# Kernel optimization log

Hardware: AMD Instinct MI355X
Metric: run time of the kernel (lower is better)

The kernel has to match this reference:

```python
import jax, jax.numpy as jnp
import numpy as np
import math

N = 512      # sequence length (residues)
CS = 384     # single_embedding_size
CZ = 128     # pair_embedding_size
C = 16       # ipa_embedding_size
PQ = 4       # num_query_points
PV = 8       # num_value_points
H = 12       # num_heads

SCALE_SINGLE = 1.0 / math.sqrt(C)
SCALE_FRAME = -1.0 / math.sqrt(18 * PQ)


def setup_inputs() -> dict:
    key = jax.random.key(0)
    ks = jax.random.split(key, 14)
    w = lambda k, shape: jax.random.normal(k, shape, dtype=jnp.float32) * 0.02
    return {
        "single_rep": jax.random.normal(ks[0], (N, CS), dtype=jnp.float32),
        "pair_rep": jax.random.normal(ks[1], (N, N, CZ), dtype=jnp.float32),
        "rotations": jax.random.normal(ks[2], (N, 3, 3), dtype=jnp.float32),
        "translations": jax.random.normal(ks[3], (N, 3), dtype=jnp.float32),
        "Wq": w(ks[4], (CS, H * C)),
        "Wk": w(ks[5], (CS, H * C)),
        "Wv": w(ks[6], (CS, H * C)),
        "Wqp": w(ks[7], (CS, H * PQ * 3)),
        "Wkp": w(ks[8], (CS, H * PQ * 3)),
        "Wvp": w(ks[9], (CS, H * PV * 3)),
        "Wb": w(ks[10], (CZ, H)),
        "Wout": w(ks[11], (H * (CZ + C + PV * 4), CS)),
        "bout": jnp.zeros((CS,), dtype=jnp.float32),
        "scale_head": jnp.ones((H,), dtype=jnp.float32),
    }


def reference(single_rep, pair_rep, rotations, translations,
              Wq, Wk, Wv, Wqp, Wkp, Wvp, Wb, Wout, bout, scale_head):
    n = single_rep.shape[0]

    def apply_frames(x):  # x: [n, h, p, 3] -> R_n x + t_n
        return jnp.einsum('nij,nhpj->nhpi', rotations, x) + translations[:, None, None, :]

    # projections
    q = (single_rep @ Wq).reshape(n, H, C)
    k = (single_rep @ Wk).reshape(n, H, C)
    v = (single_rep @ Wv).reshape(n, H, C)
    qp = (single_rep @ Wqp).reshape(n, H, PQ, 3)
    kp = (single_rep @ Wkp).reshape(n, H, PQ, 3)
    vp = (single_rep @ Wvp).reshape(n, H, PV, 3)

    # single-rep weight: [n, H, n]
    w_single = SCALE_SINGLE * jnp.einsum('nhc,mhc->nhm', q, k)

    # pair-rep bias weight: [n, H, n]
    w_pair = jnp.einsum('nmz,zh->nhm', pair_rep, Wb)

    # frame (point) weight
    lq = apply_frames(qp)  # [n,H,PQ,3]
    lk = apply_frames(kp)  # [n,H,PQ,3]
    diff = lq[:, None] - lk[None, :]                 # [n,n,H,PQ,3]
    d2 = jnp.sum(diff * diff, axis=(-1, -2))         # [n,n,H]
    w_frame = SCALE_FRAME * jax.nn.softplus(scale_head)[None, :, None] \
              * jnp.transpose(d2, (0, 2, 1))         # [n,H,n]

    weight = jax.nn.softmax(w_single + w_pair + w_frame, axis=-1)  # [n,H,n]

    # attentions
    o_single = jnp.einsum('nhm,mhc->nhc', weight, v)            # [n,H,C]
    o_pair = jnp.einsum('nhm,nmz->nhz', weight, pair_rep)       # [n,H,CZ]

    lvp = apply_frames(vp)                                      # [n,H,PV,3]
    o_local = jnp.einsum('nhm,mhpc->nhpc', weight, lvp)         # [n,H,PV,3]
    # inverse frame: R^T (x - t)
    o_frame = jnp.einsum('nji,nhpj->nhpi', rotations,
                         o_local - translations[:, None, None, :])  # [n,H,PV,3]
    o_norm = jnp.linalg.norm(o_frame, axis=-1)                  # [n,H,PV]

    att = jnp.concatenate(
        [o_single, o_pair, o_frame.reshape(n, H, PV * 3), o_norm], axis=-1)
    return att.reshape(n, -1) @ Wout + bout
```

## Files before the change

### kernel.cpp

```cpp
#include <hip/hip_runtime.h>
#include <math.h>

#define NRES 512
#define CSZ  384
#define CZ   128
#define CC   16
#define PQ   4
#define PV   8
#define NH   12

#define HC    (NH*CC)
#define HPQ3  (NH*PQ*3)
#define HPV3  (NH*PV*3)
#define ATTD  (NH*(CZ+CC+PV*4))

#define OFF_Q   0
#define OFF_K   (OFF_Q  + NRES*HC)
#define OFF_V   (OFF_K  + NRES*HC)
#define OFF_LQ  (OFF_V  + NRES*HC)
#define OFF_LK  (OFF_LQ + NRES*HPQ3)
#define OFF_LVP (OFF_LK + NRES*HPQ3)
#define OFF_ATT (OFF_LVP+ NRES*HPV3)
#define OFF_LOG (OFF_ATT + NRES*ATTD)
#define OFF_PART OFF_LOG
#define LOG_FLOATS (NRES*NH*NRES)

#define OFF_KH  OFF_ATT
#define OFF_QH  (OFF_ATT + NH*NRES*32)

#define SCALE_SINGLE 0.25f
#define SCALE_FRAME  (-0.1178511301977579f)

#define LROW 516
#define ZP   516

#define PJ_BM 32
#define PJ_BN 64
#define PJ_BK 32
#define PJ_NK (CSZ/PJ_BK)
#define PJ_AP 388

__global__ __launch_bounds__(256) void k_proj2(
    const float* __restrict__ S,
    const float* __restrict__ Wq, const float* __restrict__ Wk,
    const float* __restrict__ Wv, const float* __restrict__ Wqp,
    const float* __restrict__ Wkp, const float* __restrict__ Wvp,
    float* __restrict__ ws)
{
  __shared__ __align__(16) float A_s[PJ_BM][PJ_AP];
  __shared__ __align__(16) float B_s[PJ_BK][PJ_BN];

  const int t  = threadIdx.x;
  const int rb = blockIdx.x / 18;
  const int cb = blockIdx.x % 18;
  const int tc = t & 15, tr = t >> 4;

  #pragma unroll
  for (int j = 0; j < 12; ++j) {
    int idx = t + j*256;
    int row = idx / 96, kq = idx % 96;
    float4 v4 = *(const float4*)(S + (size_t)(rb*PJ_BM + row)*CSZ + kq*4);
    *(float4*)&A_s[row][kq*4] = v4;
  }

  const float* Wp[2]; int ncB[2], lcB[2], kkB[2], cqB[2];
  #pragma unroll
  for (int j = 0; j < 2; ++j) {
    int idx = t + j*256;
    int kk = idx >> 4, cq = idx & 15;
    kkB[j] = kk; cqB[j] = cq;
    int col = cb*PJ_BN + cq*4;
    if      (col < 192) { Wp[j]=Wq;  ncB[j]=192; lcB[j]=col;     }
    else if (col < 384) { Wp[j]=Wk;  ncB[j]=192; lcB[j]=col-192; }
    else if (col < 576) { Wp[j]=Wv;  ncB[j]=192; lcB[j]=col-384; }
    else if (col < 720) { Wp[j]=Wqp; ncB[j]=144; lcB[j]=col-576; }
    else if (col < 864) { Wp[j]=Wkp; ncB[j]=144; lcB[j]=col-720; }
    else                { Wp[j]=Wvp; ncB[j]=288; lcB[j]=col-864; }
  }

  float4 bw[2];
  #pragma unroll
  for (int j = 0; j < 2; ++j)
    bw[j] = *(const float4*)(Wp[j] + (size_t)kkB[j]*ncB[j] + lcB[j]);

  float acc[2][4];
  #pragma unroll
  for (int i=0;i<2;i++)
    #pragma unroll
    for (int jj=0;jj<4;jj++) acc[i][jj]=0.f;

  for (int ki = 0; ki < PJ_NK; ++ki) {
    __syncthreads();
    #pragma unroll
    for (int j = 0; j < 2; ++j)
      *(float4*)&B_s[kkB[j]][cqB[j]*4] = bw[j];
    __syncthreads();

    if (ki + 1 < PJ_NK) {
      #pragma unroll
      for (int j = 0; j < 2; ++j)
        bw[j] = *(const float4*)(Wp[j] + (size_t)((ki+1)*PJ_BK + kkB[j])*ncB[j] + lcB[j]);
    }

    #pragma unroll
    for (int kk4 = 0; kk4 < PJ_BK/4; ++kk4) {
      float4 a0 = *(const float4*)&A_s[tr*2+0][ki*PJ_BK + kk4*4];
      float4 a1 = *(const float4*)&A_s[tr*2+1][ki*PJ_BK + kk4*4];
      const float* a0p = (const float*)&a0;
      const float* a1p = (const float*)&a1;
      #pragma unroll
      for (int e = 0; e < 4; ++e) {
        float4 b4 = *(const float4*)&B_s[kk4*4+e][tc*4];
        float f0 = a0p[e], f1 = a1p[e];
        acc[0][0] += f0*b4.x; acc[0][1] += f0*b4.y; acc[0][2] += f0*b4.z; acc[0][3] += f0*b4.w;
        acc[1][0] += f1*b4.x; acc[1][1] += f1*b4.y; acc[1][2] += f1*b4.z; acc[1][3] += f1*b4.w;
      }
    }
  }

  {
    int col = cb*PJ_BN + tc*4;
    float* dst; int stride; int lcc;
    if      (col < 192) { dst = ws+OFF_Q;   stride=192; lcc=col;     }
    else if (col < 384) { dst = ws+OFF_K;   stride=192; lcc=col-192; }
    else if (col < 576) { dst = ws+OFF_V;   stride=192; lcc=col-384; }
    else if (col < 720) { dst = ws+OFF_LQ;  stride=144; lcc=col-576; }
    else if (col < 864) { dst = ws+OFF_LK;  stride=144; lcc=col-720; }
    else                { dst = ws+OFF_LVP; stride=288; lcc=col-864; }
    #pragma unroll
    for (int i = 0; i < 2; ++i) {
      int row = rb*PJ_BM + tr*2 + i;
      *(float4*)&dst[(size_t)row*stride + lcc] =
          make_float4(acc[i][0], acc[i][1], acc[i][2], acc[i][3]);
    }
  }
}

__global__ __launch_bounds__(256) void k_frames(
    const float* __restrict__ rot, const float* __restrict__ trans,
    float* __restrict__ ws)
{
  int gid = blockIdx.x*256 + threadIdx.x;
  if (gid >= NRES*192) return;
  int m = gid / 192;
  int rest = gid % 192;
  float* base; int pidx;
  if      (rest <  48) { base = ws + OFF_LQ  + (size_t)m*HPQ3; pidx = rest;     }
  else if (rest <  96) { base = ws + OFF_LK  + (size_t)m*HPQ3; pidx = rest-48;  }
  else                 { base = ws + OFF_LVP + (size_t)m*HPV3; pidx = rest-96;  }
  float x = base[pidx*3+0], y = base[pidx*3+1], z = base[pidx*3+2];
  const float* R = rot + (size_t)m*9;
  const float* T = trans + (size_t)m*3;
  float o0 = R[0]*x + R[1]*y + R[2]*z + T[0];
  float o1 = R[3]*x + R[4]*y + R[5]*z + T[1];
  float o2 = R[6]*x + R[7]*y + R[8]*z + T[2];
  base[pidx*3+0]=o0; base[pidx*3+1]=o1; base[pidx*3+2]=o2;
}

__global__ __launch_bounds__(256) void k_hat(
    const float* __restrict__ scale_head, float* __restrict__ ws)
{
  const int r = blockIdx.x;
  const int t = threadIdx.x;
  __shared__ float sSp[NH];
  if (t < NH) { float x = scale_head[t];
                sSp[t] = (x > 20.f) ? x : log1pf(__expf(x)); }
  __syncthreads();

  for (int i = t; i < NH*32; i += 256) {
    const int h = i >> 5, j = i & 31;
    const float* kk = ws + OFF_K  + (size_t)r*HC   + h*CC;
    const float* lk = ws + OFF_LK + (size_t)r*HPQ3 + h*12;
    const float* qq = ws + OFF_Q  + (size_t)r*HC   + h*CC;
    const float* lq = ws + OFF_LQ + (size_t)r*HPQ3 + h*12;
    float kv, qv;
    if (j < 16)      { kv = kk[j];    qv = SCALE_SINGLE * qq[j]; }
    else if (j < 28) { kv = lk[j-16]; qv = -2.f*SCALE_FRAME*sSp[h]*lq[j-16]; }
    else if (j == 28) {
      float s2 = 0.f;
      #pragma unroll
      for (int e=0;e<12;e++) { float v = lk[e]; s2 += v*v; }
      kv = SCALE_FRAME * sSp[h] * s2;
      qv = 1.f;
    } else { kv = 0.f; qv = 0.f; }
    ws[OFF_KH + ((size_t)h*NRES + r)*32 + j] = kv;
    ws[OFF_QH + ((size_t)h*NRES + r)*32 + j] = qv;
  }
}

#define QK_P 68
__global__ __launch_bounds__(256) void k_qk(float* __restrict__ ws)
{
  __shared__ __align__(16) float Qs[32*QK_P];
  __shared__ __align__(16) float Ks[32*QK_P];

  const int bid = blockIdx.x;
  const int h  = bid >> 6;
  const int nt = (bid >> 3) & 7;
  const int mt = bid & 7;
  const int t  = threadIdx.x;
  const int tc = t & 15, tr = t >> 4;

  const float4* qsrc = (const float4*)(ws + OFF_QH + ((size_t)h*NRES + nt*64)*32);
  const float4* ksrc = (const float4*)(ws + OFF_KH + ((size_t)h*NRES + mt*64)*32);

  #pragma unroll
  for (int u = 0; u < 2; ++u) {
    int idx = t + u*256;
    int r = idx >> 3, j4 = idx & 7;
    float4 qv = qsrc[idx];
    float4 kv = ksrc[idx];
    Qs[(j4*4+0)*QK_P + r] = qv.x;
    Qs[(j4*4+1)*QK_P + r] = qv.y;
    Qs[(j4*4+2)*QK_P + r] = qv.z;
    Qs[(j4*4+3)*QK_P + r] = qv.w;
    Ks[(j4*4+0)*QK_P + r] = kv.x;
    Ks[(j4*4+1)*QK_P + r] = kv.y;
    Ks[(j4*4+2)*QK_P + r] = kv.z;
    Ks[(j4*4+3)*QK_P + r] = kv.w;
  }
  __syncthreads();

  float acc[4][4];
  #pragma unroll
  for (int i=0;i<4;i++)
    #pragma unroll
    for (int k2=0;k2<4;k2++) acc[i][k2]=0.f;

  #pragma unroll
  for (int j = 0; j < 32; ++j) {
    float4 qv = *(const float4*)&Qs[j*QK_P + tr*4];
    float4 kv = *(const float4*)&Ks[j*QK_P + tc*4];
    acc[0][0] += qv.x*kv.x; acc[0][1] += qv.x*kv.y; acc[0][2] += qv.x*kv.z; acc[0][3] += qv.x*kv.w;
    acc[1][0] += qv.y*kv.x; acc[1][1] += qv.y*kv.y; acc[1][2] += qv.y*kv.z; acc[1][3] += qv.y*kv.w;
    acc[2][0] += qv.z*kv.x; acc[2][1] += qv.z*kv.y; acc[2][2] += qv.z*kv.z; acc[2][3] += qv.z*kv.w;
    acc[3][0] += qv.w*kv.x; acc[3][1] += qv.w*kv.y; acc[3][2] += qv.w*kv.z; acc[3][3] += qv.w*kv.w;
  }

  float* wlog = ws + OFF_LOG;
  #pragma unroll
  for (int i = 0; i < 4; ++i) {
    int n = nt*64 + tr*4 + i;
    *(float4*)&wlog[((size_t)n*NH + h)*NRES + mt*64 + tc*4] =
        make_float4(acc[i][0], acc[i][1], acc[i][2], acc[i][3]);
  }
}

__global__ __launch_bounds__(512) void k_attn2(
    const float* __restrict__ pair,
    const float* __restrict__ rot, const float* __restrict__ trans,
    const float* __restrict__ Wb,
    float* __restrict__ ws)
{
  const int n = blockIdx.x;
  const int t = threadIdx.x;

  __shared__ __align__(16) float sLogit[NH*LROW];
  __shared__ __align__(16) float sU[16*ZP];
  __shared__ __align__(16) float sOL[HPV3];
  __shared__ float sR[9];
  __shared__ float sT[3];

  const float* v    = ws + OFF_V;
  const float* lvp  = ws + OFF_LVP;
  const float* wlog = ws + OFF_LOG;
  float* att = ws + OFF_ATT;

  if (t >= 488 && t < 497)      sR[t-488] = rot[(size_t)n*9 + (t-488)];
  else if (t >= 497 && t < 500) sT[t-497] = trans[(size_t)n*3 + (t-497)];

  {
    float acch[NH];
    #pragma unroll
    for (int h=0;h<NH;h++)
      acch[h] = wlog[((size_t)n*NH + h)*NRES + t];

    const float4* pr4 = (const float4*)(pair + (size_t)n*NRES*CZ);

    float4 c0 = pr4[(size_t)((t +    0) >> 2)*32 + 0*4 + (t & 3)];
    float4 c1 = pr4[(size_t)((t +  512) >> 2)*32 + 0*4 + (t & 3)];
    float4 c2 = pr4[(size_t)((t + 1024) >> 2)*32 + 0*4 + (t & 3)];
    float4 c3 = pr4[(size_t)((t + 1536) >> 2)*32 + 0*4 + (t & 3)];

    #pragma unroll 1
    for (int zc = 0; zc < 8; ++zc) {
      __syncthreads();
      {
#define WR_J(CJ, J)                                                   \
        { int idx = t + (J)*512;                                      \
          int row = idx >> 2, q = idx & 3;                            \
          sU[(q*4+0)*ZP + row] = CJ.x;                                \
          sU[(q*4+1)*ZP + row] = CJ.y;                                \
          sU[(q*4+2)*ZP + row] = CJ.z;                                \
          sU[(q*4+3)*ZP + row] = CJ.w; }
        WR_J(c0, 0) WR_J(c1, 1) WR_J(c2, 2) WR_J(c3, 3)
#undef WR_J
      }
      if (zc < 7) {
        c0 = pr4[(size_t)((t +    0) >> 2)*32 + (zc+1)*4 + (t & 3)];
        c1 = pr4[(size_t)((t +  512) >> 2)*32 + (zc+1)*4 + (t & 3)];
        c2 = pr4[(size_t)((t + 1024) >> 2)*32 + (zc+1)*4 + (t & 3)];
        c3 = pr4[(size_t)((t + 1536) >> 2)*32 + (zc+1)*4 + (t & 3)];
      }
      __syncthreads();
      #pragma unroll
      for (int e = 0; e < 16; ++e) {
        float pv = sU[e*ZP + t];
        const float* wrow = Wb + (size_t)(zc*16 + e)*NH;
        #pragma unroll
        for (int h=0;h<NH;h++) acch[h] += pv * wrow[h];
      }
    }
    #pragma unroll
    for (int h=0;h<NH;h++) sLogit[h*LROW + t] = acch[h];
  }
  __syncthreads();

  {
    int wave = t >> 6, lane = t & 63;
    for (int h = wave; h < NH; h += 8) {
      float x[8]; float mx = -1e30f;
      #pragma unroll
      for (int j=0;j<8;j++) { x[j] = sLogit[h*LROW + lane + j*64]; mx = fmaxf(mx, x[j]); }
      #pragma unroll
      for (int d=1; d<64; d<<=1) mx = fmaxf(mx, __shfl_xor(mx, d, 64));
      float s = 0.f;
      #pragma unroll
      for (int j=0;j<8;j++) { x[j] = __expf(x[j]-mx); s += x[j]; }
      #pragma unroll
      for (int d=1; d<64; d<<=1) s += __shfl_xor(s, d, 64);
      float inv = 1.f/s;
      #pragma unroll
      for (int j=0;j<8;j++) sLogit[h*LROW + lane + j*64] = x[j]*inv;
    }
  }
  __syncthreads();

  {
    const int zq = t & 31;
    const int hg = (t >> 5) & 3;
    const int mg = t >> 7;
    float a0[4] = {0,0,0,0}, a1[4] = {0,0,0,0}, a2[4] = {0,0,0,0};
    const float* pb = pair + (size_t)n*NRES*CZ + zq*4;
    for (int mb = 0; mb < 32; ++mb) {
      int m0 = mg*128 + mb*4;
      float4 w0 = *(const float4*)&sLogit[(hg+0)*LROW + m0];
      float4 w1 = *(const float4*)&sLogit[(hg+4)*LROW + m0];
      float4 w2 = *(const float4*)&sLogit[(hg+8)*LROW + m0];
      const float* w0p = (const float*)&w0;
      const float* w1p = (const float*)&w1;
      const float* w2p = (const float*)&w2;
      #pragma unroll
      for (int i=0;i<4;i++) {
        float4 p4 = *(const float4*)(pb + (size_t)(m0+i)*CZ);
        const float* pp = (const float*)&p4;
        float f0 = w0p[i], f1 = w1p[i], f2 = w2p[i];
        #pragma unroll
        for (int e=0;e<4;e++) {
          a0[e] += f0*pp[e]; a1[e] += f1*pp[e]; a2[e] += f2*pp[e];
        }
      }
    }
    *(float4*)&sU[mg*(NH*CZ) + (hg+0)*CZ + zq*4] = make_float4(a0[0],a0[1],a0[2],a0[3]);
    *(float4*)&sU[mg*(NH*CZ) + (hg+4)*CZ + zq*4] = make_float4(a1[0],a1[1],a1[2],a1[3]);
    *(float4*)&sU[mg*(NH*CZ) + (hg+8)*CZ + zq*4] = make_float4(a2[0],a2[1],a2[2],a2[3]);
  }

  {
    if (t < 480) {
      float acc = 0.f;
      const float* src; int stride; int off; int h;
      if (t < 192) { h = t >> 4;        src = v;   stride = HC;   off = t;      }
      else         { int idx = t - 192; h = idx/24; src = lvp; stride = HPV3; off = idx; }
      const float* wrow = sLogit + h*LROW;
      for (int m0 = 0; m0 < NRES; m0 += 4) {
        float4 w4 = *(const float4*)&wrow[m0];
        acc += w4.x * src[(size_t)(m0+0)*stride + off];
        acc += w4.y * src[(size_t)(m0+1)*stride + off];
        acc += w4.z * src[(size_t)(m0+2)*stride + off];
        acc += w4.w * src[(size_t)(m0+3)*stride + off];
      }
      if (t < 192) {
        int h2 = t >> 4;
        att[(size_t)n*ATTD + h2*176 + (t & 15)] = acc;
      } else {
        sOL[t-192] = acc;
      }
    }
  }
  __syncthreads();

  for (int o = t; o < NH*CZ; o += 512) {
    float sres = sU[0*(NH*CZ) + o] + sU[1*(NH*CZ) + o]
               + sU[2*(NH*CZ) + o] + sU[3*(NH*CZ) + o];
    int h = o >> 7, z = o & 127;
    att[(size_t)n*ATTD + h*176 + 16 + z] = sres;
  }

  if (t < 96) {
    int h = t / 8, p = t % 8;
    float x = sOL[h*24 + p*3 + 0] - sT[0];
    float y = sOL[h*24 + p*3 + 1] - sT[1];
    float z = sOL[h*24 + p*3 + 2] - sT[2];
    float o0 = sR[0]*x + sR[3]*y + sR[6]*z;
    float o1 = sR[1]*x + sR[4]*y + sR[7]*z;
    float o2 = sR[2]*x + sR[5]*y + sR[8]*z;
    float nm = sqrtf(o0*o0 + o1*o1 + o2*o2);
    float* ab = att + (size_t)n*ATTD + h*176;
    ab[144 + p*3 + 0] = o0;
    ab[144 + p*3 + 1] = o1;
    ab[144 + p*3 + 2] = o2;
    ab[168 + p] = nm;
  }
}

__global__ __launch_bounds__(512) void k_attn(
    const float* __restrict__ pair,
    const float* __restrict__ rot, const float* __restrict__ trans,
    const float* __restrict__ Wb, const float* __restrict__ scale_head,
    float* __restrict__ ws)
{
  const int n = blockIdx.x;
  const int t = threadIdx.x;

  __shared__ __align__(16) float sLogit[NH*LROW];
  __shared__ __align__(16) float sOP[4][NH*CZ];
  __shared__ __align__(16) float sQ[HC];
  __shared__ __align__(16) float sLQ[HPQ3];
  __shared__ float sSp[NH];
  __shared__ __align__(16) float sOL[HPV3];
  __shared__ float sR[9];
  __shared__ float sT[3];

  const float* q   = ws + OFF_Q;
  const float* k   = ws + OFF_K;
  const float* v   = ws + OFF_V;
  const float* lq  = ws + OFF_LQ;
  const float* lk  = ws + OFF_LK;
  const float* lvp = ws + OFF_LVP;
  float* att = ws + OFF_ATT;

  if (t < 192)               sQ[t]      = q[(size_t)n*HC + t];
  else if (t < 336)          sLQ[t-192] = lq[(size_t)n*HPQ3 + (t-192)];
  else if (t < 348) { float x = scale_head[t-336];
                      sSp[t-336] = (x > 20.f) ? x : log1pf(__expf(x)); }
  else if (t < 357)          sR[t-348]  = rot[(size_t)n*9 + (t-348)];
  else if (t < 360)          sT[t-357]  = trans[(size_t)n*3 + (t-357)];
  __syncthreads();

  {
    const int m = t;
    float acch[NH];
    #pragma unroll
    for (int h=0;h<NH;h++) acch[h]=0.f;

    const float4* pr = (const float4*)(pair + ((size_t)n*NRES + m)*CZ);
    for (int zq = 0; zq < CZ/4; ++zq) {
      float4 p4 = pr[zq];
      const float* pp = (const float*)&p4;
      #pragma unroll
      for (int e=0;e<4;e++) {
        float pv_ = pp[e];
        const float* wrow = Wb + (size_t)(zq*4+e)*NH;
        #pragma unroll
        for (int h=0;h<NH;h++) acch[h] += pv_ * wrow[h];
      }
    }

    #pragma unroll
    for (int h=0;h<NH;h++) {
      const float4* kr = (const float4*)(k + (size_t)m*HC + h*CC);
      const float* qrow = sQ + h*CC;
      float d = 0.f;
      #pragma unroll
      for (int j=0;j<4;j++) {
        float4 k4 = kr[j];
        d += k4.x*qrow[j*4+0] + k4.y*qrow[j*4+1] + k4.z*qrow[j*4+2] + k4.w*qrow[j*4+3];
      }
      acch[h] += SCALE_SINGLE * d;

      const float* lkr = lk + (size_t)m*HPQ3 + h*12;
      const float* lqr = sLQ + h*12;
      float d2 = 0.f;
      #pragma unroll
      for (int j=0;j<12;j++) { float df = lqr[j]-lkr[j]; d2 += df*df; }
      acch[h] += SCALE_FRAME * sSp[h] * d2;

      sLogit[h*LROW + m] = acch[h];
    }
  }
  __syncthreads();

  {
    int wave = t >> 6, lane = t & 63;
    for (int h = wave; h < NH; h += 8) {
      float x[8]; float mx = -1e30f;
      #pragma unroll
      for (int j=0;j<8;j++) { x[j] = sLogit[h*LROW + lane + j*64]; mx = fmaxf(mx, x[j]); }
      #pragma unroll
      for (int d=1; d<64; d<<=1) mx = fmaxf(mx, __shfl_xor(mx, d, 64));
      float s = 0.f;
      #pragma unroll
      for (int j=0;j<8;j++) { x[j] = __expf(x[j]-mx); s += x[j]; }
      #pragma unroll
      for (int d=1; d<64; d<<=1) s += __shfl_xor(s, d, 64);
      float inv = 1.f/s;
      #pragma unroll
      for (int j=0;j<8;j++) sLogit[h*LROW + lane + j*64] = x[j]*inv;
    }
  }
  __syncthreads();

  {
    const int zq = t & 31;
    const int hg = (t >> 5) & 3;
    const int mg = t >> 7;
    float a0[4] = {0,0,0,0}, a1[4] = {0,0,0,0}, a2[4] = {0,0,0,0};
    const float* pb = pair + (size_t)n*NRES*CZ + zq*4;
    for (int mb = 0; mb < 32; ++mb) {
      int m0 = mg*128 + mb*4;
      float4 w0 = *(const float4*)&sLogit[(hg+0)*LROW + m0];
      float4 w1 = *(const float4*)&sLogit[(hg+4)*LROW + m0];
      float4 w2 = *(const float4*)&sLogit[(hg+8)*LROW + m0];
      const float* w0p = (const float*)&w0;
      const float* w1p = (const float*)&w1;
      const float* w2p = (const float*)&w2;
      #pragma unroll
      for (int i=0;i<4;i++) {
        float4 p4 = *(const float4*)(pb + (size_t)(m0+i)*CZ);
        const float* pp = (const float*)&p4;
        float f0 = w0p[i], f1 = w1p[i], f2 = w2p[i];
        #pragma unroll
        for (int e=0;e<4;e++) {
          a0[e] += f0*pp[e]; a1[e] += f1*pp[e]; a2[e] += f2*pp[e];
        }
      }
    }
    *(float4*)&sOP[mg][(hg+0)*CZ + zq*4] = make_float4(a0[0],a0[1],a0[2],a0[3]);
    *(float4*)&sOP[mg][(hg+4)*CZ + zq*4] = make_float4(a1[0],a1[1],a1[2],a1[3]);
    *(float4*)&sOP[mg][(hg+8)*CZ + zq*4] = make_float4(a2[0],a2[1],a2[2],a2[3]);
  }

  {
    if (t < 480) {
      float acc = 0.f;
      const float* src; int stride; int off; int h;
      if (t < 192) { h = t >> 4;        src = v;   stride = HC;   off = t;      }
      else         { int idx = t - 192; h = idx/24; src = lvp; stride = HPV3; off = idx; }
      const float* wrow = sLogit + h*LROW;
      for (int m0 = 0; m0 < NRES; m0 += 4) {
        float4 w4 = *(const float4*)&wrow[m0];
        acc += w4.x * src[(size_t)(m0+0)*stride + off];
        acc += w4.y * src[(size_t)(m0+1)*stride + off];
        acc += w4.z * src[(size_t)(m0+2)*stride + off];
        acc += w4.w * src[(size_t)(m0+3)*stride + off];
      }
      if (t < 192) {
        int h2 = t >> 4;
        att[(size_t)n*ATTD + h2*176 + (t & 15)] = acc;
      } else {
        sOL[t-192] = acc;
      }
    }
  }
  __syncthreads();

  for (int o = t; o < NH*CZ; o += 512) {
    float sres = sOP[0][o] + sOP[1][o] + sOP[2][o] + sOP[3][o];
    int h = o >> 7, z = o & 127;
    att[(size_t)n*ATTD + h*176 + 16 + z] = sres;
  }

  if (t < 96) {
    int h = t / 8, p = t % 8;
    float x = sOL[h*24 + p*3 + 0] - sT[0];
    float y = sOL[h*24 + p*3 + 1] - sT[1];
    float z = sOL[h*24 + p*3 + 2] - sT[2];
    float o0 = sR[0]*x + sR[3]*y + sR[6]*z;
    float o1 = sR[1]*x + sR[4]*y + sR[7]*z;
    float o2 = sR[2]*x + sR[5]*y + sR[8]*z;
    float nm = sqrtf(o0*o0 + o1*o1 + o2*o2);
    float* ab = att + (size_t)n*ATTD + h*176;
    ab[144 + p*3 + 0] = o0;
    ab[144 + p*3 + 1] = o1;
    ab[144 + p*3 + 2] = o2;
    ab[168 + p] = nm;
  }
}

#define KOUT_BK 24

__global__ __launch_bounds__(256) void k_out_part(
    const float* __restrict__ ws, const float* __restrict__ Wout,
    float* __restrict__ part, int KS)
{
  const float* att = ws + OFF_ATT;
  const int bid  = blockIdx.x;
  const int ks   = bid / 48;
  const int tile = bid % 48;
  const int rb   = tile / 6, cb = tile % 6;
  const int KLEN = ATTD / KS;
  const int k0b  = ks * KLEN;

  __shared__ __align__(16) float A_s[64][KOUT_BK+1];
  __shared__ __align__(16) float B_s[KOUT_BK][64];

  const int t  = threadIdx.x;
  const int tc = t & 15, tr = t >> 4;

  float acc[4][4];
  #pragma unroll
  for (int i=0;i<4;i++)
    #pragma unroll
    for (int j=0;j<4;j++) acc[i][j]=0.f;

  for (int k0 = k0b; k0 < k0b + KLEN; k0 += KOUT_BK) {
    __syncthreads();
    #pragma unroll
    for (int j = 0; j < 6; ++j) {
      int idx = t + j*256;
      int r  = idx / KOUT_BK, kk = idx % KOUT_BK;
      A_s[r][kk] = att[(size_t)(rb*64 + r)*ATTD + k0 + kk];
      int kk2 = idx >> 6, c = idx & 63;
      B_s[kk2][c] = Wout[(size_t)(k0 + kk2)*CSZ + cb*64 + c];
    }
    __syncthreads();
    #pragma unroll
    for (int kk = 0; kk < KOUT_BK; ++kk) {
      float4 b4 = *(const float4*)&B_s[kk][tc*4];
      float a0 = A_s[tr*4+0][kk];
      float a1 = A_s[tr*4+1][kk];
      float a2 = A_s[tr*4+2][kk];
      float a3 = A_s[tr*4+3][kk];
      acc[0][0] += a0*b4.x; acc[0][1] += a0*b4.y; acc[0][2] += a0*b4.z; acc[0][3] += a0*b4.w;
      acc[1][0] += a1*b4.x; acc[1][1] += a1*b4.y; acc[1][2] += a1*b4.z; acc[1][3] += a1*b4.w;
      acc[2][0] += a2*b4.x; acc[2][1] += a2*b4.y; acc[2][2] += a2*b4.z; acc[2][3] += a2*b4.w;
      acc[3][0] += a3*b4.x; acc[3][1] += a3*b4.y; acc[3][2] += a3*b4.z; acc[3][3] += a3*b4.w;
    }
  }

  float* pb = part + (size_t)ks*NRES*CSZ;
  #pragma unroll
  for (int i=0;i<4;i++) {
    int row = rb*64 + tr*4 + i;
    int col = cb*64 + tc*4;
    *(float4*)&pb[(size_t)row*CSZ + col] =
        make_float4(acc[i][0], acc[i][1], acc[i][2], acc[i][3]);
  }
}

__global__ __launch_bounds__(256) void k_out_reduce(
    const float* __restrict__ part, const float* __restrict__ bout,
    float* __restrict__ out, int KS)
{
  int idx4 = blockIdx.x*256 + threadIdx.x;
  if (idx4 >= NRES*CSZ/4) return;
  int c4 = idx4 % (CSZ/4);
  float4 s = ((const float4*)bout)[c4];
  const float4* p4 = (const float4*)part;
  for (int ks = 0; ks < KS; ++ks) {
    float4 v = p4[(size_t)ks*(NRES*CSZ/4) + idx4];
    s.x += v.x; s.y += v.y; s.z += v.z; s.w += v.w;
  }
  ((float4*)out)[idx4] = s;
}

__global__ __launch_bounds__(256) void k_out_v1(
    const float* __restrict__ ws, const float* __restrict__ Wout,
    const float* __restrict__ bout, float* __restrict__ out)
{
  const float* att = ws + OFF_ATT;
  int cb = blockIdx.x % 6;
  int rb = blockIdx.x / 6;
  int t  = threadIdx.x;
  int c  = cb*64 + (t & 63);
  int rg = t >> 6;
  int r0 = rb*16;
  float acc[4] = {0.f,0.f,0.f,0.f};
  for (int a = 0; a < ATTD; ++a) {
    float wv = Wout[(size_t)a*CSZ + c];
    #pragma unroll
    for (int i=0;i<4;i++)
      acc[i] += att[(size_t)(r0 + rg + 4*i)*ATTD + a] * wv;
  }
  float b = bout[c];
  #pragma unroll
  for (int i=0;i<4;i++)
    out[(size_t)(r0 + rg + 4*i)*CSZ + c] = acc[i] + b;
}

extern "C" void kernel_launch(void* const* d_in, const int* in_sizes, int n_in,
                              void* d_out, int out_size, void* d_ws, size_t ws_size,
                              hipStream_t stream) {
  const float* S     = (const float*)d_in[0];
  const float* pair  = (const float*)d_in[1];
  const float* rot   = (const float*)d_in[2];
  const float* trans = (const float*)d_in[3];
  const float* Wq    = (const float*)d_in[4];
  const float* Wk    = (const float*)d_in[5];
  const float* Wv    = (const float*)d_in[6];
  const float* Wqp   = (const float*)d_in[7];
  const float* Wkp   = (const float*)d_in[8];
  const float* Wvp   = (const float*)d_in[9];
  const float* Wb    = (const float*)d_in[10];
  const float* Wout  = (const float*)d_in[11];
  const float* bout  = (const float*)d_in[12];
  const float* sh    = (const float*)d_in[13];
  float* out = (float*)d_out;
  float* ws  = (float*)d_ws;

  hipLaunchKernelGGL(k_proj2,  dim3(16*18), dim3(256), 0, stream,
                     S, Wq, Wk, Wv, Wqp, Wkp, Wvp, ws);
  hipLaunchKernelGGL(k_frames, dim3((NRES*192+255)/256), dim3(256), 0, stream,
                     rot, trans, ws);

  const size_t need_new = (size_t)(OFF_LOG + LOG_FLOATS) * sizeof(float);
  if (ws_size >= need_new) {
    hipLaunchKernelGGL(k_hat,   dim3(NRES), dim3(256), 0, stream, sh, ws);
    hipLaunchKernelGGL(k_qk,    dim3(NH*64), dim3(256), 0, stream, ws);
    hipLaunchKernelGGL(k_attn2, dim3(NRES), dim3(512), 0, stream,
                       pair, rot, trans, Wb, ws);
  } else {
    hipLaunchKernelGGL(k_attn,  dim3(NRES), dim3(512), 0, stream,
                       pair, rot, trans, Wb, sh, ws);
  }

  int KS = 0;
  const int cands[4] = {8, 4, 2, 1};
  for (int i = 0; i < 4; ++i) {
    size_t need = ((size_t)OFF_PART + (size_t)cands[i]*NRES*CSZ) * sizeof(float);
    if (need <= ws_size) { KS = cands[i]; break; }
  }
  if (KS > 0) {
    hipLaunchKernelGGL(k_out_part, dim3(48*KS), dim3(256), 0, stream,
                       ws, Wout, ws + OFF_PART, KS);
    hipLaunchKernelGGL(k_out_reduce, dim3((NRES*CSZ/4 + 255)/256), dim3(256), 0, stream,
                       ws + OFF_PART, bout, out, KS);
  } else {
    hipLaunchKernelGGL(k_out_v1, dim3(32*6), dim3(256), 0, stream,
                       ws, Wout, bout, out);
  }
}
```

Measured before the change: 146.0 us.

## Split attention kernel across two blocks per residue by head halves

Each residue's attention block is split into two blocks, each handling six of the twelve heads, doubling the grid size. This is meant to raise occupancy and parallelism, with a smaller shared-memory footprint per block. In exchange, each block re-reads the full pair-representation row, doubling pair_rep global traffic unless the second read hits in cache. The pair-weighted reduction is restructured into eight row groups instead of four.

```diff
diff --git a/kernel.cpp b/kernel.cpp
--- a/kernel.cpp
+++ b/kernel.cpp
@@ -252,12 +252,14 @@
     const float* __restrict__ Wb,
     float* __restrict__ ws)
 {
-  const int n = blockIdx.x;
-  const int t = threadIdx.x;
-
-  __shared__ __align__(16) float sLogit[NH*LROW];
+  const int n    = blockIdx.x >> 1;
+  const int half = blockIdx.x & 1;
+  const int h0   = half*6;
+  const int t    = threadIdx.x;
+
+  __shared__ __align__(16) float sLogit[6*LROW];
   __shared__ __align__(16) float sU[16*ZP];
-  __shared__ __align__(16) float sOL[HPV3];
+  __shared__ __align__(16) float sOL[6*PV*3];
   __shared__ float sR[9];
   __shared__ float sT[3];
 
@@ -270,10 +272,10 @@
   else if (t >= 497 && t < 500) sT[t-497] = trans[(size_t)n*3 + (t-497)];
 
   {
-    float acch[NH];
-    #pragma unroll
-    for (int h=0;h<NH;h++)
-      acch[h] = wlog[((size_t)n*NH + h)*NRES + t];
+    float acch[6];
+    #pragma unroll
+    for (int h=0;h<6;h++)
+      acch[h] = wlog[((size_t)n*NH + h0 + h)*NRES + t];
 
     const float4* pr4 = (const float4*)(pair + (size_t)n*NRES*CZ);
 
@@ -306,19 +308,20 @@
       #pragma unroll
       for (int e = 0; e < 16; ++e) {
         float pv = sU[e*ZP + t];
-        const float* wrow = Wb + (size_t)(zc*16 + e)*NH;
+        const float* wrow = Wb + (size_t)(zc*16 + e)*NH + h0;
         #pragma unroll
-        for (int h=0;h<NH;h++) acch[h] += pv * wrow[h];
-      }
-    }
-    #pragma unroll
-    for (int h=0;h<NH;h++) sLogit[h*LROW + t] = acch[h];
+        for (int h=0;h<6;h++) acch[h] += pv * wrow[h];
+      }
+    }
+    #pragma unroll
+    for (int h=0;h<6;h++) sLogit[h*LROW + t] = acch[h];
   }
   __syncthreads();
 
   {
     int wave = t >> 6, lane = t & 63;
-    for (int h = wave; h < NH; h += 8) {
+    if (wave < 6) {
+      int h = wave;
       float x[8]; float mx = -1e30f;
       #pragma unroll
       for (int j=0;j<8;j++) { x[j] = sLogit[h*LROW + lane + j*64]; mx = fmaxf(mx, x[j]); }
@@ -338,15 +341,15 @@
 
   {
     const int zq = t & 31;
-    const int hg = (t >> 5) & 3;
-    const int mg = t >> 7;
+    const int hg = (t >> 5) & 1;
+    const int mg = t >> 6;
     float a0[4] = {0,0,0,0}, a1[4] = {0,0,0,0}, a2[4] = {0,0,0,0};
     const float* pb = pair + (size_t)n*NRES*CZ + zq*4;
-    for (int mb = 0; mb < 32; ++mb) {
-      int m0 = mg*128 + mb*4;
-      float4 w0 = *(const float4*)&sLogit[(hg+0)*LROW + m0];
-      float4 w1 = *(const float4*)&sLogit[(hg+4)*LROW + m0];
-      float4 w2 = *(const float4*)&sLogit[(hg+8)*LROW + m0];
+    for (int mb = 0; mb < 16; ++mb) {
+      int m0 = mg*64 + mb*4;
+      float4 w0 = *(const float4*)&sLogit[(hg*3+0)*LROW + m0];
+      float4 w1 = *(const float4*)&sLogit[(hg*3+1)*LROW + m0];
+      float4 w2 = *(const float4*)&sLogit[(hg*3+2)*LROW + m0];
       const float* w0p = (const float*)&w0;
       const float* w1p = (const float*)&w1;
       const float* w2p = (const float*)&w2;
@@ -361,18 +364,20 @@
         }
       }
     }
-    *(float4*)&sU[mg*(NH*CZ) + (hg+0)*CZ + zq*4] = make_float4(a0[0],a0[1],a0[2],a0[3]);
-    *(float4*)&sU[mg*(NH*CZ) + (hg+4)*CZ + zq*4] = make_float4(a1[0],a1[1],a1[2],a1[3]);
-    *(float4*)&sU[mg*(NH*CZ) + (hg+8)*CZ + zq*4] = make_float4(a2[0],a2[1],a2[2],a2[3]);
-  }
-
-  {
-    if (t < 480) {
+    *(float4*)&sU[mg*(6*CZ) + (hg*3+0)*CZ + zq*4] = make_float4(a0[0],a0[1],a0[2],a0[3]);
+    *(float4*)&sU[mg*(6*CZ) + (hg*3+1)*CZ + zq*4] = make_float4(a1[0],a1[1],a1[2],a1[3]);
+    *(float4*)&sU[mg*(6*CZ) + (hg*3+2)*CZ + zq*4] = make_float4(a2[0],a2[1],a2[2],a2[3]);
+  }
+
+  {
+    if (t < 240) {
       float acc = 0.f;
-      const float* src; int stride; int off; int h;
-      if (t < 192) { h = t >> 4;        src = v;   stride = HC;   off = t;      }
-      else         { int idx = t - 192; h = idx/24; src = lvp; stride = HPV3; off = idx; }
-      const float* wrow = sLogit + h*LROW;
+      const float* src; int stride; int off; int lh;
+      if (t < 96) { lh = t >> 4;        src = v;   stride = HC;
+                    off = (h0 + lh)*CC + (t & 15); }
+      else        { int idx = t - 96;   lh = idx/24; src = lvp; stride = HPV3;
+                    off = h0*24 + idx; }
+      const float* wrow = sLogit + lh*LROW;
       for (int m0 = 0; m0 < NRES; m0 += 4) {
         float4 w4 = *(const float4*)&wrow[m0];
         acc += w4.x * src[(size_t)(m0+0)*stride + off];
@@ -380,33 +385,33 @@
         acc += w4.z * src[(size_t)(m0+2)*stride + off];
         acc += w4.w * src[(size_t)(m0+3)*stride + off];
       }
-      if (t < 192) {
-        int h2 = t >> 4;
-        att[(size_t)n*ATTD + h2*176 + (t & 15)] = acc;
+      if (t < 96) {
+        att[(size_t)n*ATTD + (h0 + lh)*176 + (t & 15)] = acc;
       } else {
-        sOL[t-192] = acc;
-      }
-    }
-  }
-  __syncthreads();
-
-  for (int o = t; o < NH*CZ; o += 512) {
-    float sres = sU[0*(NH*CZ) + o] + sU[1*(NH*CZ) + o]
-               + sU[2*(NH*CZ) + o] + sU[3*(NH*CZ) + o];
-    int h = o >> 7, z = o & 127;
-    att[(size_t)n*ATTD + h*176 + 16 + z] = sres;
-  }
-
-  if (t < 96) {
-    int h = t / 8, p = t % 8;
-    float x = sOL[h*24 + p*3 + 0] - sT[0];
-    float y = sOL[h*24 + p*3 + 1] - sT[1];
-    float z = sOL[h*24 + p*3 + 2] - sT[2];
+        sOL[t-96] = acc;
+      }
+    }
+  }
+  __syncthreads();
+
+  for (int o = t; o < 6*CZ; o += 512) {
+    float sres = 0.f;
+    #pragma unroll
+    for (int mg = 0; mg < 8; ++mg) sres += sU[mg*(6*CZ) + o];
+    int lh = o >> 7, z = o & 127;
+    att[(size_t)n*ATTD + (h0 + lh)*176 + 16 + z] = sres;
+  }
+
+  if (t < 48) {
+    int lh = t / 8, p = t % 8;
+    float x = sOL[lh*24 + p*3 + 0] - sT[0];
+    float y = sOL[lh*24 + p*3 + 1] - sT[1];
+    float z = sOL[lh*24 + p*3 + 2] - sT[2];
     float o0 = sR[0]*x + sR[3]*y + sR[6]*z;
     float o1 = sR[1]*x + sR[4]*y + sR[7]*z;
     float o2 = sR[2]*x + sR[5]*y + sR[8]*z;
     float nm = sqrtf(o0*o0 + o1*o1 + o2*o2);
-    float* ab = att + (size_t)n*ATTD + h*176;
+    float* ab = att + (size_t)n*ATTD + (h0 + lh)*176;
     ab[144 + p*3 + 0] = o0;
     ab[144 + p*3 + 1] = o1;
     ab[144 + p*3 + 2] = o2;
@@ -718,7 +723,7 @@
   if (ws_size >= need_new) {
     hipLaunchKernelGGL(k_hat,   dim3(NRES), dim3(256), 0, stream, sh, ws);
     hipLaunchKernelGGL(k_qk,    dim3(NH*64), dim3(256), 0, stream, ws);
-    hipLaunchKernelGGL(k_attn2, dim3(NRES), dim3(512), 0, stream,
+    hipLaunchKernelGGL(k_attn2, dim3(NRES*2), dim3(512), 0, stream,
                        pair, rot, trans, Wb, ws);
   } else {
     hipLaunchKernelGGL(k_attn,  dim3(NRES), dim3(512), 0, stream,
```

Result: slower. 205.7 us (+40.9%).
